# Kernel tuning notes

Measured on AMD Instinct MI355X. Metric: run time of the kernel, lower is better.

## Reference

```python
import jax, jax.numpy as jnp
import numpy as np


def setup_inputs() -> dict:
    key = jax.random.key(0)
    k1, k2, k3, k4, k5 = jax.random.split(key, 5)
    B, S, I, O, R = 4, 2048, 4096, 4096, 16
    s = 1.0 / np.sqrt(I)
    return {
        "x": jax.random.normal(k1, (B, S, I), dtype=jnp.float32),
        "W": jax.random.normal(k2, (O, I), dtype=jnp.float32) * s,
        "b": jax.random.normal(k3, (O,), dtype=jnp.float32) * 0.02,
        "lora_A": jax.random.normal(k4, (I, R), dtype=jnp.float32) * s,
        "lora_B": jax.random.normal(k5, (R, O), dtype=jnp.float32) * 0.02,
    }


def reference(x, W, b, lora_A, lora_B):
    # Base linear: F.linear(x, W, b) = x @ W.T + b   -> [B, S, O]
    base_out = jnp.einsum("bsi,oi->bso", x, W) + b
    # LoRA low-rank delta: (x @ A) @ B  -> [B, S, O]
    lora_out = jnp.einsum("bsr,ro->bso", jnp.einsum("bsi,ir->bsr", x, lora_A), lora_B)
    return base_out + lora_out
```

## Files before the change

### kernel.cpp

```cpp
#include <hip/hip_runtime.h>

typedef float f32x4 __attribute__((ext_vector_type(4)));
typedef __bf16 bf16x8 __attribute__((ext_vector_type(8)));
typedef __bf16 bf16x4 __attribute__((ext_vector_type(4)));

#define GLOBAL_AS __attribute__((address_space(1)))
#define LDS_AS    __attribute__((address_space(3)))

static __device__ __forceinline__ void gload16(const void* g, void* l) {
  __builtin_amdgcn_global_load_lds((const GLOBAL_AS void*)g, (LDS_AS void*)l, 16, 0, 0);
}

#define BAR() __builtin_amdgcn_s_barrier()
#define WAITL0() do { asm volatile("s_waitcnt lgkmcnt(0)" ::: "memory"); __builtin_amdgcn_sched_barrier(0); } while (0)

__global__ __launch_bounds__(256)
void xa_cvt(const float* __restrict__ X, const float* __restrict__ A,
            __bf16* __restrict__ Xb, __bf16* __restrict__ XAb) {
  constexpr int K = 4096, TM = 16, KC = 64;
  __shared__ float Xs[TM][68];
  __shared__ float At[16][68];
  const int t = threadIdx.x;
  const int m0 = blockIdx.x * TM;
  const int lrow = t >> 4, c4 = (t & 15) * 4;
  const int orow = t >> 4, oc = t & 15;
  const int akk = t >> 2, ar4 = (t & 3) * 4;
  f32x4 av = (f32x4)0.f;
  for (int k0 = 0; k0 < K; k0 += KC) {
    const float* gx = X + (size_t)(m0 + lrow) * K + k0 + c4;
    f32x4 u = *reinterpret_cast<const f32x4*>(gx);
    *reinterpret_cast<f32x4*>(&Xs[lrow][c4]) = u;
    bf16x4 p;
#pragma unroll
    for (int e = 0; e < 4; ++e) p[e] = (__bf16)u[e];
    *reinterpret_cast<bf16x4*>(Xb + (size_t)(m0 + lrow) * K + k0 + c4) = p;
    f32x4 a = *reinterpret_cast<const f32x4*>(A + (size_t)(k0 + akk) * 16 + ar4);
    At[ar4 + 0][akk] = a[0]; At[ar4 + 1][akk] = a[1];
    At[ar4 + 2][akk] = a[2]; At[ar4 + 3][akk] = a[3];
    __syncthreads();
#pragma unroll
    for (int q = 0; q < 16; ++q) {
      f32x4 xv = *reinterpret_cast<const f32x4*>(&Xs[orow][q * 4]);
      av += xv * *reinterpret_cast<const f32x4*>(&At[oc][q * 4]);
    }
    __syncthreads();
  }
  const float acc = av[0] + av[1] + av[2] + av[3];
  const size_t base = (size_t)(m0 + orow) * 64;
  XAb[base + oc] = (__bf16)acc;
#pragma unroll
  for (int z = 0; z < 3; ++z) XAb[base + 16 + z * 16 + oc] = (__bf16)0.f;
}

__global__ __launch_bounds__(256)
void cvt_f32_bf16(const float* __restrict__ in, __bf16* __restrict__ out, long n8) {
  long i = (long)blockIdx.x * blockDim.x + threadIdx.x;
  long stride = (long)gridDim.x * blockDim.x;
  for (; i < n8; i += stride) {
    f32x4 u = reinterpret_cast<const f32x4*>(in)[2 * i];
    f32x4 v = reinterpret_cast<const f32x4*>(in)[2 * i + 1];
    bf16x8 p;
#pragma unroll
    for (int e = 0; e < 4; ++e) { p[e] = (__bf16)u[e]; p[4 + e] = (__bf16)v[e]; }
    reinterpret_cast<bf16x8*>(out)[i] = p;
  }
}

__global__ __launch_bounds__(256)
void blt64(const float* __restrict__ Bl, __bf16* __restrict__ BlT) {
  int idx = blockIdx.x * 256 + threadIdx.x;
  int col = idx >> 6, k = idx & 63;
  float v = (k < 16) ? Bl[(size_t)k * 4096 + col] : 0.f;
  BlT[idx] = (__bf16)v;
}

__global__ __launch_bounds__(512, 2)
void gemm8(const __bf16* __restrict__ Xb, const __bf16* __restrict__ Wb,
           const __bf16* __restrict__ XAb, const __bf16* __restrict__ BlT,
           const float* __restrict__ bias, float* __restrict__ out) {
  constexpr int N = 4096, K = 4096;
  __shared__ __align__(16) char sm[131072];
  char* Asm_ = sm;
  char* Bsm_ = sm + 65536;

  const int t = threadIdx.x;
  const int lane = t & 63, w = t >> 6;
  const int wr = w >> 2, wc = w & 3;
  const int fr = lane & 15, fg = lane >> 4;

  const int bid = blockIdx.x;
  const int xcd = bid & 7, l = bid >> 3;
  const int mt = (xcd << 2) | ((l >> 4) & 2) | (l & 1);
  const int nt = (l >> 1) & 15;
  const int m0 = mt * 256, n0 = nt * 256;

  const int sRow = w * 16 + (lane >> 2);
  const int sColB = (((lane & 3) ^ ((lane >> 3) & 3)) << 4);
  const int rdOff = fr * 64 + ((fg ^ ((fr >> 1) & 3)) << 4);
  const int rdOffA = wr * 16384 + rdOff;
  const int rdOffB = (wc >> 1) * 16384 + (wc & 1) * 8192 + rdOff;

  auto stageA = [&](int h, int tt) {
    char* dst = Asm_ + (tt & 1) * 32768 + h * 16384 + w * 2048;
    const char* g;
    if (tt < 64) g = (const char*)(Xb + (size_t)(m0 + h * 128 + sRow) * K + (size_t)tt * 64) + sColB;
    else         g = (const char*)(XAb + (size_t)(m0 + h * 128 + sRow) * 64) + sColB;
    gload16(g, dst);
    gload16(g + 64, dst + 1024);
  };
  auto stageB = [&](int h, int tt) {
    char* dst = Bsm_ + (tt & 1) * 32768 + h * 16384 + w * 2048;
    const char* g;
    if (tt < 64) g = (const char*)(Wb + (size_t)(n0 + h * 128 + sRow) * K + (size_t)tt * 64) + sColB;
    else         g = (const char*)(BlT + (size_t)(n0 + h * 128 + sRow) * 64) + sColB;
    gload16(g, dst);
    gload16(g + 64, dst + 1024);
  };

  auto rdA = [&](int b, int mf, int kk) -> bf16x8 {
    return *reinterpret_cast<const bf16x8*>(Asm_ + b * 32768 + (mf * 2 + kk) * 1024 + rdOffA);
  };
  auto rdB = [&](int b, int nf, int kk) -> bf16x8 {
    return *reinterpret_cast<const bf16x8*>(Bsm_ + b * 32768 + (nf * 2 + kk) * 1024 + rdOffB);
  };

  f32x4 acc[8][4];
#pragma unroll
  for (int i = 0; i < 8; ++i)
#pragma unroll
    for (int j = 0; j < 4; ++j) acc[i][j] = (f32x4)0.f;

  bf16x8 aF[4][2], bL[2][2], bH[2][2];

  auto MF = [&](bf16x8 (&af)[4][2], bf16x8 (&bf_)[2][2], int mi, int ni) {
#pragma unroll
    for (int i = 0; i < 4; ++i)
#pragma unroll
      for (int j = 0; j < 2; ++j)
#pragma unroll
        for (int kk = 0; kk < 2; ++kk)
          acc[mi * 4 + i][ni * 2 + j] = __builtin_amdgcn_mfma_f32_16x16x32_bf16(
              af[i][kk], bf_[j][kk], acc[mi * 4 + i][ni * 2 + j], 0, 0, 0);
  };

  auto tile_step = [&](int tv) {
    const int b = tv & 1;
#pragma unroll
    for (int i = 0; i < 4; ++i)
#pragma unroll
      for (int kk = 0; kk < 2; ++kk) aF[i][kk] = rdA(b, i, kk);
#pragma unroll
    for (int j = 0; j < 2; ++j)
#pragma unroll
      for (int kk = 0; kk < 2; ++kk) bL[j][kk] = rdB(b, j, kk);
    stageA(1, tv + 1);
    BAR(); WAITL0();
    __builtin_amdgcn_s_setprio(1); MF(aF, bL, 0, 0); __builtin_amdgcn_s_setprio(0);
    BAR();
#pragma unroll
    for (int j = 0; j < 2; ++j)
#pragma unroll
      for (int kk = 0; kk < 2; ++kk) bH[j][kk] = rdB(b, 2 + j, kk);
    BAR(); WAITL0();
    __builtin_amdgcn_s_setprio(1); MF(aF, bH, 0, 1); __builtin_amdgcn_s_setprio(0);
    BAR();
#pragma unroll
    for (int i = 0; i < 4; ++i)
#pragma unroll
      for (int kk = 0; kk < 2; ++kk) aF[i][kk] = rdA(b, 4 + i, kk);
    stageB(0, tv + 2);
    BAR(); WAITL0();
    __builtin_amdgcn_s_setprio(1); MF(aF, bH, 1, 1); __builtin_amdgcn_s_setprio(0);
    BAR();
    stageB(1, tv + 2);
    stageA(0, tv + 2);
    BAR(); WAITL0();
    __builtin_amdgcn_s_setprio(1); MF(aF, bL, 1, 0); __builtin_amdgcn_s_setprio(0);
    asm volatile("s_waitcnt vmcnt(6)" ::: "memory");
    BAR();
  };

  stageA(0, 0); stageA(1, 0); stageB(0, 0); stageB(1, 0);
  stageB(0, 1); stageB(1, 1); stageA(0, 1);
  asm volatile("s_waitcnt vmcnt(6)" ::: "memory");
  BAR();

  for (int tv = 0; tv < 63; ++tv) tile_step(tv);

  {
    const int b = 1;
#pragma unroll
    for (int i = 0; i < 4; ++i)
#pragma unroll
      for (int kk = 0; kk < 2; ++kk) aF[i][kk] = rdA(b, i, kk);
#pragma unroll
    for (int j = 0; j < 2; ++j)
#pragma unroll
      for (int kk = 0; kk < 2; ++kk) bL[j][kk] = rdB(b, j, kk);
    stageA(1, 64);
    BAR(); WAITL0();
    __builtin_amdgcn_s_setprio(1); MF(aF, bL, 0, 0); __builtin_amdgcn_s_setprio(0);
    BAR();
#pragma unroll
    for (int j = 0; j < 2; ++j)
#pragma unroll
      for (int kk = 0; kk < 2; ++kk) bH[j][kk] = rdB(b, 2 + j, kk);
    BAR(); WAITL0();
    __builtin_amdgcn_s_setprio(1); MF(aF, bH, 0, 1); __builtin_amdgcn_s_setprio(0);
    BAR();
#pragma unroll
    for (int i = 0; i < 4; ++i)
#pragma unroll
      for (int kk = 0; kk < 2; ++kk) aF[i][kk] = rdA(b, 4 + i, kk);
    BAR(); WAITL0();
    __builtin_amdgcn_s_setprio(1); MF(aF, bH, 1, 1); __builtin_amdgcn_s_setprio(0);
    BAR();
    __builtin_amdgcn_s_setprio(1); MF(aF, bL, 1, 0); __builtin_amdgcn_s_setprio(0);
    asm volatile("s_waitcnt vmcnt(0)" ::: "memory");
    BAR();
  }

  {
#pragma unroll
    for (int i = 0; i < 4; ++i)
#pragma unroll
      for (int kk = 0; kk < 2; ++kk) aF[i][kk] = rdA(0, i, kk);
#pragma unroll
    for (int j = 0; j < 2; ++j)
#pragma unroll
      for (int kk = 0; kk < 2; ++kk) { bL[j][kk] = rdB(0, j, kk); bH[j][kk] = rdB(0, 2 + j, kk); }
    MF(aF, bL, 0, 0); MF(aF, bH, 0, 1);
#pragma unroll
    for (int i = 0; i < 4; ++i)
#pragma unroll
      for (int kk = 0; kk < 2; ++kk) aF[i][kk] = rdA(0, 4 + i, kk);
    MF(aF, bH, 1, 1); MF(aF, bL, 1, 0);
  }

  float bb[4];
#pragma unroll
  for (int j = 0; j < 4; ++j) bb[j] = bias[n0 + wc * 64 + j * 16 + fr];
#pragma unroll
  for (int i = 0; i < 8; ++i) {
    const int row0 = m0 + wr * 128 + i * 16 + fg * 4;
#pragma unroll
    for (int j = 0; j < 4; ++j) {
      const int col = n0 + wc * 64 + j * 16 + fr;
#pragma unroll
      for (int q = 0; q < 4; ++q)
        out[(size_t)(row0 + q) * N + col] = acc[i][j][q] + bb[j];
    }
  }
}

extern "C" void kernel_launch(void* const* d_in, const int* in_sizes, int n_in,
                              void* d_out, int out_size, void* d_ws, size_t ws_size,
                              hipStream_t stream) {
  const float* x  = (const float*)d_in[0];
  const float* W  = (const float*)d_in[1];
  const float* b  = (const float*)d_in[2];
  const float* lA = (const float*)d_in[3];
  const float* lB = (const float*)d_in[4];
  float* out = (float*)d_out;

  char* ws = (char*)d_ws;
  __bf16* Xb  = (__bf16*)ws;
  __bf16* Wb  = (__bf16*)(ws + 67108864);
  __bf16* XAb = (__bf16*)(ws + 100663296);
  __bf16* BlT = (__bf16*)(ws + 101711872);

  xa_cvt<<<8192 / 16, 256, 0, stream>>>(x, lA, Xb, XAb);
  cvt_f32_bf16<<<1024, 256, 0, stream>>>(W, Wb, (long)4096 * 4096 / 8);
  blt64<<<4096 * 64 / 256, 256, 0, stream>>>(lB, BlT);

  gemm8<<<dim3(512), dim3(512), 0, stream>>>(Xb, Wb, XAb, BlT, b, out);
}
```

Baseline: 336.4 us.

## Restage A-tile prefetch into the current tile step and fold epilogue into loop

Moves both A-half prefetches for the next tile into the first two phases of each tile step, instead of splitting them across the current and previous step. B prefetch stays two tiles ahead and is guarded at the tail, so the separate peeled last-tile block is removed and the loop runs 64 steps unrolled by two. The vmcnt waits drop from 6 to 4 and a partial lgkmcnt wait is added, changing how LDS reads overlap with global-to-LDS loads. The aim is a more regular software pipeline with less issue overhead. The risk is a shorter prefetch distance for A, which may expose more global latency, and it relies on the reworked wait counts being correct.

```diff
diff --git a/kernel.cpp b/kernel.cpp
--- a/kernel.cpp
+++ b/kernel.cpp
@@ -153,73 +153,42 @@
     for (int j = 0; j < 2; ++j)
 #pragma unroll
       for (int kk = 0; kk < 2; ++kk) bL[j][kk] = rdB(b, j, kk);
+    stageA(0, tv + 1);
+    asm volatile("s_waitcnt lgkmcnt(8)" ::: "memory");
+    BAR(); WAITL0();
+    __builtin_amdgcn_s_setprio(1); MF(aF, bL, 0, 0); __builtin_amdgcn_s_setprio(0);
+    BAR();
+#pragma unroll
+    for (int j = 0; j < 2; ++j)
+#pragma unroll
+      for (int kk = 0; kk < 2; ++kk) bH[j][kk] = rdB(b, 2 + j, kk);
     stageA(1, tv + 1);
     BAR(); WAITL0();
-    __builtin_amdgcn_s_setprio(1); MF(aF, bL, 0, 0); __builtin_amdgcn_s_setprio(0);
-    BAR();
-#pragma unroll
-    for (int j = 0; j < 2; ++j)
-#pragma unroll
-      for (int kk = 0; kk < 2; ++kk) bH[j][kk] = rdB(b, 2 + j, kk);
-    BAR(); WAITL0();
     __builtin_amdgcn_s_setprio(1); MF(aF, bH, 0, 1); __builtin_amdgcn_s_setprio(0);
     BAR();
 #pragma unroll
     for (int i = 0; i < 4; ++i)
 #pragma unroll
       for (int kk = 0; kk < 2; ++kk) aF[i][kk] = rdA(b, 4 + i, kk);
-    stageB(0, tv + 2);
+    if (tv + 2 <= 64) stageB(0, tv + 2);
     BAR(); WAITL0();
     __builtin_amdgcn_s_setprio(1); MF(aF, bH, 1, 1); __builtin_amdgcn_s_setprio(0);
     BAR();
-    stageB(1, tv + 2);
-    stageA(0, tv + 2);
+    if (tv + 2 <= 64) stageB(1, tv + 2);
     BAR(); WAITL0();
     __builtin_amdgcn_s_setprio(1); MF(aF, bL, 1, 0); __builtin_amdgcn_s_setprio(0);
-    asm volatile("s_waitcnt vmcnt(6)" ::: "memory");
-    BAR();
-  };
-
-  stageA(0, 0); stageA(1, 0); stageB(0, 0); stageB(1, 0);
-  stageB(0, 1); stageB(1, 1); stageA(0, 1);
-  asm volatile("s_waitcnt vmcnt(6)" ::: "memory");
+    asm volatile("s_waitcnt vmcnt(4)" ::: "memory");
+    BAR();
+  };
+
+  stageA(0, 0); stageA(1, 0); stageB(0, 0); stageB(1, 0); stageB(0, 1); stageB(1, 1);
+  asm volatile("s_waitcnt vmcnt(4)" ::: "memory");
   BAR();
 
-  for (int tv = 0; tv < 63; ++tv) tile_step(tv);
-
-  {
-    const int b = 1;
-#pragma unroll
-    for (int i = 0; i < 4; ++i)
-#pragma unroll
-      for (int kk = 0; kk < 2; ++kk) aF[i][kk] = rdA(b, i, kk);
-#pragma unroll
-    for (int j = 0; j < 2; ++j)
-#pragma unroll
-      for (int kk = 0; kk < 2; ++kk) bL[j][kk] = rdB(b, j, kk);
-    stageA(1, 64);
-    BAR(); WAITL0();
-    __builtin_amdgcn_s_setprio(1); MF(aF, bL, 0, 0); __builtin_amdgcn_s_setprio(0);
-    BAR();
-#pragma unroll
-    for (int j = 0; j < 2; ++j)
-#pragma unroll
-      for (int kk = 0; kk < 2; ++kk) bH[j][kk] = rdB(b, 2 + j, kk);
-    BAR(); WAITL0();
-    __builtin_amdgcn_s_setprio(1); MF(aF, bH, 0, 1); __builtin_amdgcn_s_setprio(0);
-    BAR();
-#pragma unroll
-    for (int i = 0; i < 4; ++i)
-#pragma unroll
-      for (int kk = 0; kk < 2; ++kk) aF[i][kk] = rdA(b, 4 + i, kk);
-    BAR(); WAITL0();
-    __builtin_amdgcn_s_setprio(1); MF(aF, bH, 1, 1); __builtin_amdgcn_s_setprio(0);
-    BAR();
-    __builtin_amdgcn_s_setprio(1); MF(aF, bL, 1, 0); __builtin_amdgcn_s_setprio(0);
-    asm volatile("s_waitcnt vmcnt(0)" ::: "memory");
-    BAR();
-  }
-
+  for (int tp = 0; tp < 32; ++tp) { tile_step(2 * tp); tile_step(2 * tp + 1); }
+
+  asm volatile("s_waitcnt vmcnt(0)" ::: "memory");
+  BAR();
   {
 #pragma unroll
     for (int i = 0; i < 4; ++i)
```

Measured after the change: 322.1 us. 1.04x faster.
